# Kernel tuning notes

Measured on AMD Instinct MI355X. Metric: run time of the kernel, lower is better.

## Reference

```python
import jax, jax.numpy as jnp
import numpy as np

N_NODES = 10000
DROP_P = 0.5


def _gcn_conv(x, row, col, W, b):
    # PyG GCNConv: add self-loops, symmetric normalization, scatter-add aggregate
    n = x.shape[0]
    loops = jnp.arange(n)
    row = jnp.concatenate([row, loops])  # src
    col = jnp.concatenate([col, loops])  # dst
    xw = x @ W  # [N, H]
    deg = jax.ops.segment_sum(jnp.ones(col.shape, dtype=xw.dtype), col, num_segments=n)
    dinv = jnp.where(deg > 0, jax.lax.rsqrt(jnp.maximum(deg, 1e-12)), 0.0)
    norm = dinv[row] * dinv[col]  # [E+N]
    msg = xw[row] * norm[:, None]  # [E+N, H]
    return jax.ops.segment_sum(msg, col, num_segments=n) + b


def setup_inputs() -> dict:
    key = jax.random.key(0)
    k1, k2, k3, k4, k5, k6 = jax.random.split(key, 6)
    B, N, E, F, H = 8, N_NODES, 320000, 128, 128
    xs = jax.random.normal(k1, (B, N, F), dtype=jnp.float32)
    edge_indexs = jax.random.randint(k2, (B, 2, E), 0, N, dtype=jnp.int64)
    s1 = 1.0 / np.sqrt(F)
    s2 = 1.0 / np.sqrt(H)
    W1 = jax.random.uniform(k3, (F, H), jnp.float32, -s1, s1)
    b1 = jnp.zeros((H,), jnp.float32)
    W2 = jax.random.uniform(k4, (H, H), jnp.float32, -s2, s2)
    b2 = jnp.zeros((H,), jnp.float32)
    return {"xs": xs, "edge_indexs": edge_indexs, "W1": W1, "b1": b1, "W2": W2, "b2": b2}


def reference(xs, edge_indexs, W1, b1, W2, b2):
    # Fixed dropout mask (F.dropout is active in the original; fixed key for determinism)
    drop_mask = jax.random.bernoulli(jax.random.key(42), 1.0 - DROP_P, (xs.shape[1], W1.shape[1]))

    def per_graph(x, ei):
        row, col = ei[0], ei[1]
        h = jax.nn.relu(_gcn_conv(x, row, col, W1, b1))
        h = jnp.where(drop_mask, h / (1.0 - DROP_P), 0.0)
        return _gcn_conv(h, row, col, W2, b2)

    return jax.vmap(per_graph)(xs, edge_indexs)
```

## Files before the change

### kernel.cpp

```cpp
#include <hip/hip_runtime.h>
#include <hip/hip_bf16.h>

#define NB 8
#define NN 10000
#define NE 320000
#define NF 128
#define NH 128
#define RNG 32
#define RS 313
#define BCAP 12288
#define NCHUNK 128
#define P1E 2500
#define P1CAP 160

typedef __attribute__((ext_vector_type(8))) _Float16 half8;
typedef __attribute__((ext_vector_type(4))) float f32x4;


__device__ __forceinline__ int load_edge_nt(const int* ei, size_t idx, int is64) {
    if (is64) return (int)__builtin_nontemporal_load(((const long long*)ei) + idx);
    return __builtin_nontemporal_load(ei + idx);
}

__device__ __forceinline__ unsigned short f2bf(float x) {
    __hip_bfloat16 h = __float2bfloat16(x);
    return *reinterpret_cast<unsigned short*>(&h);
}

__device__ __forceinline__ void bf8_add(float* a, uint4 u) {
    union { unsigned q; float f; } t;
    t.q = u.x << 16;         a[0] += t.f;
    t.q = u.x & 0xffff0000u; a[1] += t.f;
    t.q = u.y << 16;         a[2] += t.f;
    t.q = u.y & 0xffff0000u; a[3] += t.f;
    t.q = u.z << 16;         a[4] += t.f;
    t.q = u.z & 0xffff0000u; a[5] += t.f;
    t.q = u.w << 16;         a[6] += t.f;
    t.q = u.w & 0xffff0000u; a[7] += t.f;
}

__global__ void detect_kernel(const int* __restrict__ ei, int* __restrict__ flag) {
    __shared__ int s;
    if (threadIdx.x == 0) s = 1;
    __syncthreads();
    int bad = 0;
    for (int q = threadIdx.x; q < 1024; q += 256)
        if (ei[2 * q + 1] != 0) bad = 1;
    if (bad) atomicAnd(&s, 0);
    __syncthreads();
    if (threadIdx.x == 0) *flag = s;
}

__global__ void mask_kernel(float* __restrict__ mask) {
    const unsigned TOT = NN * NH;
    unsigned i = blockIdx.x * 256 + threadIdx.x;
    if (i >= TOT) return;
    const unsigned ks0 = 0u, ks1 = 42u, ks2 = 0x1BD11BDAu ^ 0u ^ 42u;
    unsigned x0 = 0u + ks0;
    unsigned x1 = i + ks1;
#define TFR(r) { x0 += x1; x1 = (x1 << (r)) | (x1 >> (32 - (r))); x1 ^= x0; }
    TFR(13) TFR(15) TFR(26) TFR(6)
    x0 += ks1; x1 += ks2 + 1u;
    TFR(17) TFR(29) TFR(16) TFR(24)
    x0 += ks2; x1 += ks0 + 2u;
    TFR(13) TFR(15) TFR(26) TFR(6)
    x0 += ks0; x1 += ks1 + 3u;
    TFR(17) TFR(29) TFR(16) TFR(24)
    x0 += ks1; x1 += ks2 + 4u;
    TFR(13) TFR(15) TFR(26) TFR(6)
    x0 += ks2; x1 += ks0 + 5u;
#undef TFR
    unsigned bits = x0 ^ x1;
    mask[i] = (bits & 0x80000000u) ? 0.0f : 2.0f;
}

__global__ __launch_bounds__(256) void part_kernel(const int* __restrict__ ei,
                                                   const int* __restrict__ flag,
                                                   int* __restrict__ counts,
                                                   unsigned* __restrict__ gbucket) {
    int b = blockIdx.x & 7;
    int chunk = blockIdx.x >> 3;
    int e0 = chunk * P1E;
    __shared__ int bcnt[RNG];
    __shared__ unsigned bbuf[RNG][P1CAP + 1];
    if (threadIdx.x < RNG) bcnt[threadIdx.x] = 0;
    __syncthreads();
    int is64 = *flag;
    size_t base = (size_t)b * 2 * NE;
    for (int e = e0 + threadIdx.x; e < e0 + P1E; e += 256) {
        int row = load_edge_nt(ei, base + e, is64);
        int col = load_edge_nt(ei, base + NE + e, is64);
        int bk = col / RS;
        unsigned pk = ((unsigned)col << 14) | (unsigned)row;
        int p = atomicAdd(&bcnt[bk], 1);
        if (p < P1CAP) bbuf[bk][p] = pk;
    }
    __syncthreads();
    if (threadIdx.x < RNG) {
        int c = bcnt[threadIdx.x];
        counts[(b * RNG + threadIdx.x) * NCHUNK + chunk] = c < P1CAP ? c : P1CAP;
    }
    int wave = threadIdx.x >> 6, lane = threadIdx.x & 63;
    for (int bk = wave; bk < RNG; bk += 4) {
        int len = bcnt[bk]; if (len > P1CAP) len = P1CAP;
        unsigned* dst = gbucket + ((size_t)(b * RNG + bk) * NCHUNK + chunk) * P1CAP;
        for (int i = lane; i < len; i += 64) dst[i] = bbuf[bk][i];
    }
}

__global__ __launch_bounds__(512) void build_kernel(const unsigned* __restrict__ gbucket,
                                                    const int* __restrict__ counts,
                                                    int* __restrict__ csr,
                                                    int* __restrict__ deg,
                                                    int* __restrict__ offs,
                                                    float* __restrict__ dinv) {
    int b = blockIdx.x & 7;
    int r = blockIdx.x >> 3;
    int n0 = r * RS;
    int nloc = (NN - n0 < RS) ? (NN - n0) : RS;
    __shared__ int lcnt[NCHUNK];
    __shared__ int cnt[512];
    __shared__ int cur[RS];
    __shared__ int buf[BCAP];
    int gidx = b * RNG + r;
    const unsigned* src = gbucket + (size_t)gidx * NCHUNK * P1CAP;
    int t = threadIdx.x;
    if (t < NCHUNK) lcnt[t] = counts[gidx * NCHUNK + t];
    cnt[t] = 0;
    __syncthreads();
    for (int idx = t; idx < NCHUNK * P1CAP; idx += 512) {
        int c = idx / P1CAP, s = idx - c * P1CAP;
        if (s < lcnt[c])
            atomicAdd(&cnt[(src[(size_t)c * P1CAP + s] >> 14) - n0], 1);
    }
    __syncthreads();
    int v = cnt[t];
    __syncthreads();
    int x = v;
    cnt[t] = x;
    __syncthreads();
    for (int off = 1; off < 512; off <<= 1) {
        int add = (t >= off) ? cnt[t - off] : 0;
        __syncthreads();
        x += add;
        cnt[t] = x;
        __syncthreads();
    }
    int K = cnt[511];
    int excl = x - v;
    if (t < nloc) {
        deg[b * NN + n0 + t] = v;
        offs[b * NN + n0 + t] = gidx * BCAP + excl;
        dinv[b * NN + n0 + t] = 1.0f / sqrtf((float)(v + 1));
        cur[t] = excl;
    }
    __syncthreads();
    for (int idx = t; idx < NCHUNK * P1CAP; idx += 512) {
        int c = idx / P1CAP, s = idx - c * P1CAP;
        if (s < lcnt[c]) {
            unsigned pk = src[(size_t)c * P1CAP + s];
            int p = atomicAdd(&cur[(pk >> 14) - n0], 1);
            if (p < BCAP) buf[p] = (int)((pk & 16383u) << 8);
        }
    }
    __syncthreads();
    int lim = K < BCAP ? K : BCAP;
    int* dstc = csr + (size_t)gidx * BCAP;
    for (int i = t; i < lim; i += 512) dstc[i] = buf[i];
}

__global__ __launch_bounds__(256) void gemm_mfma(const float* __restrict__ X,
                                                 const float* __restrict__ Wm,
                                                 const float* __restrict__ dinv,
                                                 unsigned short* __restrict__ y) {
    __shared__ _Float16 WT[128][136];
    int b = blockIdx.x & 7;
    int row0 = (blockIdx.x >> 3) * 64;
    int t = threadIdx.x;
    for (int e = t; e < 16384; e += 256) {
        int k = e >> 7, c = e & 127;
        WT[c][k] = (_Float16)Wm[e];
    }
    __syncthreads();

    int lane = t & 63;
    int wrow = row0 + (t >> 6) * 16;
    int r = lane & 15;
    int g = lane >> 4;
    const float* Xb = X + (size_t)b * NN * NF;
    int grow = wrow + r;

    f32x4 acc[8] = {};
#pragma unroll
    for (int kk = 0; kk < 4; ++kk) {
        half8 a;
        if (grow < NN) {
            const float* px = Xb + (size_t)grow * NF + kk * 32 + g * 8;
            float4 x0 = *(const float4*)px;
            float4 x1 = *(const float4*)(px + 4);
            a[0] = (_Float16)x0.x; a[1] = (_Float16)x0.y;
            a[2] = (_Float16)x0.z; a[3] = (_Float16)x0.w;
            a[4] = (_Float16)x1.x; a[5] = (_Float16)x1.y;
            a[6] = (_Float16)x1.z; a[7] = (_Float16)x1.w;
        } else {
            a = (half8)(_Float16)0.0f;
        }
#pragma unroll
        for (int c = 0; c < 8; ++c) {
            half8 bf = *(const half8*)&WT[c * 16 + r][kk * 32 + g * 8];
            acc[c] = __builtin_amdgcn_mfma_f32_16x16x32_f16(a, bf, acc[c], 0, 0, 0);
        }
    }

#pragma unroll
    for (int i = 0; i < 4; ++i) {
        int orow = wrow + g * 4 + i;
        if (orow >= NN) continue;
        float d = dinv[b * NN + orow];
        unsigned short* yp = y + ((size_t)b * NN + orow) * NH + r;
#pragma unroll
        for (int c = 0; c < 8; ++c)
            yp[c * 16] = f2bf(acc[c][i] * d);
    }
}

template<int LAYER>
__global__ __launch_bounds__(256) void aggregate_full(const unsigned short* __restrict__ y,
                                                      const int* __restrict__ offs,
                                                      const int* __restrict__ deg,
                                                      const int* __restrict__ csr,
                                                      const float* __restrict__ dinv,
                                                      const float* __restrict__ bias,
                                                      const float* __restrict__ mask,
                                                      float* __restrict__ out) {
    int b = blockIdx.x & 7;
    int w = threadIdx.x >> 6;
    int idx = (blockIdx.x >> 3) * 4 + w;
    int n0 = idx, n1 = idx + 5000;
    int lane = threadIdx.x & 63;
    int q = lane >> 4;
    unsigned q16 = (unsigned)(lane & 15) * 16u;
    const char* ybc = (const char*)(y + (size_t)b * NN * NH);

    float a0[8] = {0.f,0.f,0.f,0.f,0.f,0.f,0.f,0.f};
    float a1[8] = {0.f,0.f,0.f,0.f,0.f,0.f,0.f,0.f};
    if (q == 0) {
        uint4 s0 = *(const uint4*)(ybc + (unsigned)n0 * 256u + q16);
        uint4 s1 = *(const uint4*)(ybc + (unsigned)n1 * 256u + q16);
        bf8_add(a0, s0);
        bf8_add(a1, s1);
    }

    const int* ob = offs + b * NN;
    const int* db = deg + b * NN;
    int ba = ob[n0], o1a = ba + db[n0];
    int bb = ob[n1], o1b = bb + db[n1];

#define PROCQ(r_, j_, acc_) { \
    unsigned o = (unsigned)__shfl((r_), (j_) + q); \
    uint4 u = *(const uint4*)(ybc + o + q16); \
    bf8_add(acc_, u); \
}
#define PROCT(r_, j_, rem_, acc_) { \
    unsigned o = (unsigned)__shfl((r_), (j_) + (q < (rem_) ? q : 0)); \
    uint4 u = *(const uint4*)(ybc + o + q16); \
    if (q < (rem_)) bf8_add(acc_, u); \
}

    while (ba < o1a || bb < o1b) {
        int ma = o1a - ba; ma = ma < 0 ? 0 : (ma > 64 ? 64 : ma);
        int mb = o1b - bb; mb = mb < 0 ? 0 : (mb > 64 ? 64 : mb);
        int ra = (lane < ma) ? csr[ba + lane] : 0;
        int rb = (lane < mb) ? csr[bb + lane] : 0;
        int mmin = ma < mb ? ma : mb;
        int jj = 0;
#pragma unroll 2
        for (; jj + 3 < mmin; jj += 4) {
            PROCQ(ra, jj, a0)
            PROCQ(rb, jj, a1)
        }
        int ja = jj, jb = jj;
#pragma unroll 2
        for (; ja + 3 < ma; ja += 4) PROCQ(ra, ja, a0)
        if (ja < ma) PROCT(ra, ja, ma - ja, a0)
#pragma unroll 2
        for (; jb + 3 < mb; jb += 4) PROCQ(rb, jb, a1)
        if (jb < mb) PROCT(rb, jb, mb - jb, a1)
        ba += 64; bb += 64;
    }
#undef PROCQ
#undef PROCT

#pragma unroll
    for (int i = 0; i < 8; ++i) {
        a0[i] += __shfl_xor(a0[i], 16);
        a0[i] += __shfl_xor(a0[i], 32);
        a1[i] += __shfl_xor(a1[i], 16);
        a1[i] += __shfl_xor(a1[i], 32);
    }

    if (q < 2) {
        int n = q ? n1 : n0;
        float av[8];
#pragma unroll
        for (int i = 0; i < 8; ++i) av[i] = q ? a1[i] : a0[i];
        float d = dinv[b * NN + n];
        unsigned f0 = (lane & 15) * 8;
        float4 bi0 = *(const float4*)(bias + f0);
        float4 bi1 = *(const float4*)(bias + f0 + 4);
        float4 o0, o1;
        o0.x = fmaf(d, av[0], bi0.x);
        o0.y = fmaf(d, av[1], bi0.y);
        o0.z = fmaf(d, av[2], bi0.z);
        o0.w = fmaf(d, av[3], bi0.w);
        o1.x = fmaf(d, av[4], bi1.x);
        o1.y = fmaf(d, av[5], bi1.y);
        o1.z = fmaf(d, av[6], bi1.z);
        o1.w = fmaf(d, av[7], bi1.w);
        if (LAYER == 1) {
            float4 m0 = *(const float4*)(mask + (size_t)n * NH + f0);
            float4 m1 = *(const float4*)(mask + (size_t)n * NH + f0 + 4);
            o0.x = fmaxf(o0.x, 0.f) * m0.x;
            o0.y = fmaxf(o0.y, 0.f) * m0.y;
            o0.z = fmaxf(o0.z, 0.f) * m0.z;
            o0.w = fmaxf(o0.w, 0.f) * m0.w;
            o1.x = fmaxf(o1.x, 0.f) * m1.x;
            o1.y = fmaxf(o1.y, 0.f) * m1.y;
            o1.z = fmaxf(o1.z, 0.f) * m1.z;
            o1.w = fmaxf(o1.w, 0.f) * m1.w;
        }
        float* op = out + ((size_t)b * NN + n) * NH + f0;
        *(float4*)op = o0;
        *(float4*)(op + 4) = o1;
    }
}

extern "C" void kernel_launch(void* const* d_in, const int* in_sizes, int n_in,
                              void* d_out, int out_size, void* d_ws, size_t ws_size,
                              hipStream_t stream) {
    const float* xs = (const float*)d_in[0];
    const int*   ei = (const int*)d_in[1];
    const float* W1 = (const float*)d_in[2];
    const float* b1 = (const float*)d_in[3];
    const float* W2 = (const float*)d_in[4];
    const float* b2 = (const float*)d_in[5];
    float* out = (float*)d_out;

    float* ws        = (float*)d_ws;
    float* dinv      = ws;
    int*   deg       = (int*)(ws + 80000);
    int*   flag      = (int*)(ws + 160000);
    float* mask      = ws + 160016;
    int*   offs      = (int*)(ws + 1440016);
    int*   counts    = (int*)(ws + 1520016);
    unsigned* gbucket= (unsigned*)(ws + 1552784);
    int*   csr       = (int*)(ws + 6795664);
    unsigned short* y= (unsigned short*)(ws + 9941392);

    detect_kernel<<<1, 256, 0, stream>>>(ei, flag);
    mask_kernel<<<(NN * NH + 255) / 256, 256, 0, stream>>>(mask);
    part_kernel<<<NB * NCHUNK, 256, 0, stream>>>(ei, flag, counts, gbucket);
    build_kernel<<<NB * RNG, 512, 0, stream>>>(gbucket, counts, csr, deg, offs, dinv);

    dim3 gemm_grid(8 * ((NN + 63) / 64));
    dim3 agg_grid(NB * (5000 / 4));

    gemm_mfma<<<gemm_grid, 256, 0, stream>>>(xs, W1, dinv, y);
    aggregate_full<1><<<agg_grid, 256, 0, stream>>>(y, offs, deg, csr, dinv, b1, mask, out);

    gemm_mfma<<<gemm_grid, 256, 0, stream>>>(out, W2, dinv, y);
    aggregate_full<2><<<agg_grid, 256, 0, stream>>>(y, offs, deg, csr, dinv, b2, nullptr, out);
}
```

Measured before the change: 181.6 us.

## Pad CSR neighbor lists to multiples of four with a zero sentinel row

Each node's CSR neighbor segment is padded to a multiple of four entries, and the padding points at an extra all-zero row appended to each graph's bf16 feature buffer. The aggregation loop then always gathers four neighbors at a time and drops the masked tail path, which removes divergent tail handling. In exchange it adds padding gathers that read the zero row, slightly more CSR capacity use (BCAP overflow risk), and a change to the y row stride.

```diff
diff --git a/kernel.cpp b/kernel.cpp
--- a/kernel.cpp
+++ b/kernel.cpp
@@ -3,6 +3,7 @@
 
 #define NB 8
 #define NN 10000
+#define NROW 10001
 #define NE 320000
 #define NF 128
 #define NH 128
@@ -12,6 +13,7 @@
 #define NCHUNK 128
 #define P1E 2500
 #define P1CAP 160
+#define ZOFF (NN << 8)
 
 typedef __attribute__((ext_vector_type(8))) _Float16 half8;
 typedef __attribute__((ext_vector_type(4))) float f32x4;
@@ -39,9 +41,15 @@
     t.q = u.w & 0xffff0000u; a[7] += t.f;
 }
 
-__global__ void detect_kernel(const int* __restrict__ ei, int* __restrict__ flag) {
+__global__ void detect_kernel(const int* __restrict__ ei, int* __restrict__ flag,
+                              unsigned short* __restrict__ y) {
     __shared__ int s;
     if (threadIdx.x == 0) s = 1;
+    for (int i = threadIdx.x; i < NB * 64; i += 256) {
+        int g = i >> 6, j = i & 63;
+        unsigned* zr = (unsigned*)(y + ((size_t)g * NROW + NN) * NH);
+        zr[j] = 0u;
+    }
     __syncthreads();
     int bad = 0;
     for (int q = threadIdx.x; q < 1024; q += 256)
@@ -135,8 +143,9 @@
     }
     __syncthreads();
     int v = cnt[t];
-    __syncthreads();
-    int x = v;
+    int vp = (v + 3) & ~3;
+    __syncthreads();
+    int x = vp;
     cnt[t] = x;
     __syncthreads();
     for (int off = 1; off < 512; off <<= 1) {
@@ -147,7 +156,7 @@
         __syncthreads();
     }
     int K = cnt[511];
-    int excl = x - v;
+    int excl = x - vp;
     if (t < nloc) {
         deg[b * NN + n0 + t] = v;
         offs[b * NN + n0 + t] = gidx * BCAP + excl;
@@ -162,6 +171,9 @@
             int p = atomicAdd(&cur[(pk >> 14) - n0], 1);
             if (p < BCAP) buf[p] = (int)((pk & 16383u) << 8);
         }
+    }
+    if (t < nloc) {
+        for (int p = excl + v; p < excl + vp && p < BCAP; ++p) buf[p] = ZOFF;
     }
     __syncthreads();
     int lim = K < BCAP ? K : BCAP;
@@ -217,7 +229,7 @@
         int orow = wrow + g * 4 + i;
         if (orow >= NN) continue;
         float d = dinv[b * NN + orow];
-        unsigned short* yp = y + ((size_t)b * NN + orow) * NH + r;
+        unsigned short* yp = y + ((size_t)b * NROW + orow) * NH + r;
 #pragma unroll
         for (int c = 0; c < 8; ++c)
             yp[c * 16] = f2bf(acc[c][i] * d);
@@ -240,7 +252,7 @@
     int lane = threadIdx.x & 63;
     int q = lane >> 4;
     unsigned q16 = (unsigned)(lane & 15) * 16u;
-    const char* ybc = (const char*)(y + (size_t)b * NN * NH);
+    const char* ybc = (const char*)(y + (size_t)b * NROW * NH);
 
     float a0[8] = {0.f,0.f,0.f,0.f,0.f,0.f,0.f,0.f};
     float a1[8] = {0.f,0.f,0.f,0.f,0.f,0.f,0.f,0.f};
@@ -253,18 +265,13 @@
 
     const int* ob = offs + b * NN;
     const int* db = deg + b * NN;
-    int ba = ob[n0], o1a = ba + db[n0];
-    int bb = ob[n1], o1b = bb + db[n1];
+    int ba = ob[n0], o1a = ba + ((db[n0] + 3) & ~3);
+    int bb = ob[n1], o1b = bb + ((db[n1] + 3) & ~3);
 
 #define PROCQ(r_, j_, acc_) { \
     unsigned o = (unsigned)__shfl((r_), (j_) + q); \
     uint4 u = *(const uint4*)(ybc + o + q16); \
     bf8_add(acc_, u); \
-}
-#define PROCT(r_, j_, rem_, acc_) { \
-    unsigned o = (unsigned)__shfl((r_), (j_) + (q < (rem_) ? q : 0)); \
-    uint4 u = *(const uint4*)(ybc + o + q16); \
-    if (q < (rem_)) bf8_add(acc_, u); \
 }
 
     while (ba < o1a || bb < o1b) {
@@ -274,22 +281,18 @@
         int rb = (lane < mb) ? csr[bb + lane] : 0;
         int mmin = ma < mb ? ma : mb;
         int jj = 0;
-#pragma unroll 2
-        for (; jj + 3 < mmin; jj += 4) {
+#pragma unroll 4
+        for (; jj < mmin; jj += 4) {
             PROCQ(ra, jj, a0)
             PROCQ(rb, jj, a1)
         }
-        int ja = jj, jb = jj;
 #pragma unroll 2
-        for (; ja + 3 < ma; ja += 4) PROCQ(ra, ja, a0)
-        if (ja < ma) PROCT(ra, ja, ma - ja, a0)
+        for (int ja = jj; ja < ma; ja += 4) PROCQ(ra, ja, a0)
 #pragma unroll 2
-        for (; jb + 3 < mb; jb += 4) PROCQ(rb, jb, a1)
-        if (jb < mb) PROCT(rb, jb, mb - jb, a1)
+        for (int jb = jj; jb < mb; jb += 4) PROCQ(rb, jb, a1)
         ba += 64; bb += 64;
     }
 #undef PROCQ
-#undef PROCT
 
 #pragma unroll
     for (int i = 0; i < 8; ++i) {
@@ -357,7 +360,7 @@
     int*   csr       = (int*)(ws + 6795664);
     unsigned short* y= (unsigned short*)(ws + 9941392);
 
-    detect_kernel<<<1, 256, 0, stream>>>(ei, flag);
+    detect_kernel<<<1, 256, 0, stream>>>(ei, flag, y);
     mask_kernel<<<(NN * NH + 255) / 256, 256, 0, stream>>>(mask);
     part_kernel<<<NB * NCHUNK, 256, 0, stream>>>(ei, flag, counts, gbucket);
     build_kernel<<<NB * RNG, 512, 0, stream>>>(gbucket, counts, csr, deg, offs, dinv);
```

Result: no change. 180.8 us (-0.4%).
